# Optimization experiments

Measured on AMD Instinct MI355X. Metric: run time of the kernel, lower is better.

The kernel has to match this reference:

```python
import jax, jax.numpy as jnp
import numpy as np

D_MODEL = 2048
N_HEADS = 16
D_K = D_MODEL // N_HEADS
BATCH = 4
SEQ = 2048


def setup_inputs() -> dict:
    key = jax.random.key(0)
    ks = jax.random.split(key, 9)
    s = 1.0 / np.sqrt(D_MODEL)
    return {
        "x": jax.random.normal(ks[0], (BATCH, SEQ, D_MODEL), dtype=jnp.float32),
        "wq_w": jax.random.normal(ks[1], (D_MODEL, D_MODEL), dtype=jnp.float32) * s,
        "wq_b": jax.random.normal(ks[2], (D_MODEL,), dtype=jnp.float32) * 0.02,
        "wk_w": jax.random.normal(ks[3], (D_MODEL, D_MODEL), dtype=jnp.float32) * s,
        "wk_b": jax.random.normal(ks[4], (D_MODEL,), dtype=jnp.float32) * 0.02,
        "wv_w": jax.random.normal(ks[5], (D_MODEL, D_MODEL), dtype=jnp.float32) * s,
        "wv_b": jax.random.normal(ks[6], (D_MODEL,), dtype=jnp.float32) * 0.02,
        "wo_w": jax.random.normal(ks[7], (D_MODEL, D_MODEL), dtype=jnp.float32) * s,
        "wo_b": jax.random.normal(ks[8], (D_MODEL,), dtype=jnp.float32) * 0.02,
    }


def reference(x, wq_w, wq_b, wk_w, wk_b, wv_w, wv_b, wo_w, wo_b):
    b, s, _ = x.shape
    # Linear projections (torch Linear: x @ W^T + b)
    def split_heads(t):  # (b, s, d_model) -> (b, h, s, d_k)
        return t.reshape(b, s, N_HEADS, D_K).transpose(0, 2, 1, 3)
    q = split_heads(x @ wq_w.T + wq_b)
    k = split_heads(x @ wk_w.T + wk_b)
    v = split_heads(x @ wv_w.T + wv_b)
    scale = 1.0 / jnp.sqrt(jnp.asarray(D_K, dtype=x.dtype))
    scores = jnp.einsum("bhqd,bhkd->bhqk", q, k) * scale  # (b, h, s, s)
    attn = jax.nn.softmax(scores, axis=-1)
    ctx = jnp.einsum("bhqk,bhkd->bhqd", attn, v)
    ctx = ctx.transpose(0, 2, 1, 3).reshape(b, s, D_MODEL)
    out = ctx @ wo_w.T + wo_b
    return out
```

## Files before the change

kernel.cpp:

```cpp
#include <hip/hip_runtime.h>
#include <hip/hip_bf16.h>
#include <math.h>

typedef __attribute__((ext_vector_type(8))) short short8;
typedef __attribute__((ext_vector_type(4))) float f32x4;
typedef __attribute__((ext_vector_type(16))) float f32x16;
typedef __attribute__((ext_vector_type(4))) unsigned short u16x4;
typedef __attribute__((ext_vector_type(8))) unsigned short u16x8;
typedef __attribute__((ext_vector_type(4))) unsigned int u32x4;
typedef __attribute__((ext_vector_type(2))) int i32x2;
typedef unsigned short u16;
typedef unsigned int u32;

#define DM 2048
#define SQ 2048
#define NB 4
#define NH 16
#define DKH 128
#define KT 64
#define NT (SQ / KT)
#define LD3 (3 * DM)
#define QSCALE (0.08838834764831845f * 1.4426950408889634f)

__device__ __forceinline__ u16 f2bf(float f) {
  unsigned u = __float_as_uint(f);
  u += 0x7fffu + ((u >> 16) & 1u);
  return (u16)(u >> 16);
}

__device__ __forceinline__ u32 cvtpk(float lo, float hi) {
  u32 r;
  asm("v_cvt_pk_bf16_f32 %0, %1, %2" : "=v"(r) : "v"(lo), "v"(hi));
  return r;
}

__device__ __forceinline__ void gload16(const u16* g, u16* lds) {
  __builtin_amdgcn_global_load_lds(
      (const __attribute__((address_space(1))) unsigned int*)g,
      (__attribute__((address_space(3))) unsigned int*)lds, 16, 0, 0);
}

__global__ void cvt_bf16(const float* __restrict__ in, u16* __restrict__ out, int n) {
  int i = (blockIdx.x * blockDim.x + threadIdx.x) * 4;
  if (i >= n) return;
  float4 v = *(const float4*)(in + i);
  u16x4 o;
  o.x = f2bf(v.x); o.y = f2bf(v.y); o.z = f2bf(v.z); o.w = f2bf(v.w);
  *(u16x4*)(out + i) = o;
}

__global__ void cvt_w4(const float* __restrict__ w0, const float* __restrict__ w1,
                       const float* __restrict__ w2, const float* __restrict__ w3,
                       u16* __restrict__ dst) {
  const int sel = blockIdx.y;
  const float* src;
  switch (sel) {
    case 0: src = w0; break;
    case 1: src = w1; break;
    case 2: src = w2; break;
    default: src = w3; break;
  }
  const int i = (blockIdx.x * blockDim.x + threadIdx.x) * 4;
  float4 v = *(const float4*)(src + i);
  u16x4 o;
  o.x = f2bf(v.x); o.y = f2bf(v.y); o.z = f2bf(v.z); o.w = f2bf(v.w);
  *(u16x4*)(dst + (size_t)sel * DM * DM + i) = o;
}


#define STG_A(T, HALF)                                                     \
  do {                                                                     \
    _Pragma("unroll") for (int uu = 0; uu < 2; ++uu) {                     \
      const int j_ = w * 2 + uu;               \
      gload16(As + (size_t)((HALF) * 128 + (j_ >> 2) * 32) * K +           \
                  (size_t)(T) * 64 + (j_ & 3) * 16,                        \
              &smA[((T) & 1) * 16384 + ((HALF) * 16 + j_) * 512]);         \
    }                                                                      \
  } while (0)

#define STG_B(T, HALF)                                                     \
  do {                                                                     \
    _Pragma("unroll") for (int uu = 0; uu < 2; ++uu) {                     \
      const int j_ = w * 2 + uu;                                           \
      gload16(Bs + (size_t)((HALF) * 128 + (j_ >> 2) * 32) * K +           \
                  (size_t)(T) * 64 + (j_ & 3) * 16,                        \
              &smB[((T) & 1) * 16384 + ((HALF) * 16 + j_) * 512]);         \
    }                                                                      \
  } while (0)

#define LDA(QM)                                                            \
  do {                                                                     \
    const int rb_ = wr * 4 + (QM) * 2;                                     \
    const u16* p_ = &smA[bi * 16384 + rb_ * 2048 + l * 8];                 \
    _Pragma("unroll") for (int s = 0; s < 4; ++s) {                        \
      af[0][s] = *(const short8*)&p_[s * 512];                             \
      af[1][s] = *(const short8*)&p_[2048 + s * 512];                      \
    }                                                                      \
  } while (0)

#define LDB(QN)                                                            \
  do {                                                                     \
    const int rb_ = wc * 2 + (QN);                                         \
    const u16* p_ = &smB[bi * 16384 + rb_ * 2048 + l * 8];                 \
    _Pragma("unroll") for (int s = 0; s < 4; ++s)                          \
      bf[QN][s] = *(const short8*)&p_[s * 512];                            \
  } while (0)

#define MFMA_Q(QM, QN)                                                             \
  __builtin_amdgcn_s_setprio(1);                                                   \
  _Pragma("unroll") for (int s = 0; s < 4; ++s) {                                  \
    acc[(QM) * 2][(QN)] = __builtin_amdgcn_mfma_f32_32x32x16_bf16(                 \
        af[0][s], bf[QN][s], acc[(QM) * 2][(QN)], 0, 0, 0);                        \
    acc[(QM) * 2 + 1][(QN)] = __builtin_amdgcn_mfma_f32_32x32x16_bf16(             \
        af[1][s], bf[QN][s], acc[(QM) * 2 + 1][(QN)], 0, 0, 0);                    \
  }                                                                                \
  __builtin_amdgcn_s_setprio(0);

#define WAIT_LGKM                                         \
  asm volatile("s_waitcnt lgkmcnt(0)" ::: "memory");      \
  __builtin_amdgcn_sched_barrier(0);

template <int MODE>
__global__ __launch_bounds__(512, 2) void gemm8p(
    const u16* __restrict__ A, const u16* __restrict__ B,
    const float* __restrict__ bq, const float* __restrict__ bk,
    const float* __restrict__ bvp, void* __restrict__ Cout,
    int M, int N, int K) {
  __shared__ u16 smA[2 * 16384];
  __shared__ u16 smB[2 * 16384];
  const int tid = threadIdx.x;
  const int w = tid >> 6, l = tid & 63;
  const int c5 = l & 31, hi = l >> 5;
  const int wr = w >> 2, wc = w & 3;

  int flat = blockIdx.x + (int)gridDim.x * (int)blockIdx.y;
  const int nwg = (int)(gridDim.x * gridDim.y);
  flat = (flat & 7) * (nwg >> 3) + (flat >> 3);
  const int m0 = (flat / (int)gridDim.x) * 256, n0 = (flat % (int)gridDim.x) * 256;

  const int NSTEP = K / 64;
  f32x16 acc[4][2] = {};

  const u16* As = A + (size_t)(m0 + c5) * K + hi * 8;
  const u16* Bs = B + (size_t)(n0 + c5) * K + hi * 8;

  STG_A(0, 0); STG_A(0, 1); STG_B(0, 0); STG_B(0, 1);
  STG_B(1, 0); STG_A(1, 0);
  asm volatile("s_waitcnt vmcnt(4)" ::: "memory");
  __builtin_amdgcn_s_barrier();

  short8 af[2][4], bf[2][4];
  for (int t = 0; t < NSTEP; ++t) {
    const int bi = t & 1;
    LDA(0); LDB(0);
    if (t + 1 < NSTEP) STG_B(t + 1, 1);
    __builtin_amdgcn_s_barrier();
    WAIT_LGKM;
    MFMA_Q(0, 0);
    __builtin_amdgcn_s_barrier();
    LDB(1);
    if (t + 1 < NSTEP) STG_A(t + 1, 1);
    __builtin_amdgcn_s_barrier();
    WAIT_LGKM;
    MFMA_Q(0, 1);
    __builtin_amdgcn_s_barrier();
    LDA(1);
    if (t + 2 < NSTEP) STG_B(t + 2, 0);
    __builtin_amdgcn_s_barrier();
    WAIT_LGKM;
    MFMA_Q(1, 1);
    __builtin_amdgcn_s_barrier();
    if (t + 2 < NSTEP) STG_A(t + 2, 0);
    __builtin_amdgcn_s_barrier();
    MFMA_Q(1, 0);
    if (t + 2 < NSTEP)
      asm volatile("s_waitcnt vmcnt(4)" ::: "memory");
    else if (t + 1 < NSTEP)
      asm volatile("s_waitcnt vmcnt(0)" ::: "memory");
    __builtin_amdgcn_s_barrier();
  }

#pragma unroll
  for (int nf = 0; nf < 2; ++nf) {
    const int col = n0 + wc * 64 + nf * 32 + c5;
    float bval, os;
    if (MODE == 0) {
      const int seg = col >> 11;
      const float* bp = seg == 0 ? bq : (seg == 1 ? bk : bvp);
      bval = bp[col & (DM - 1)];
      os = (seg == 0) ? QSCALE : 1.0f;
    } else {
      bval = bq[col];
      os = 1.0f;
    }
#pragma unroll
    for (int mf = 0; mf < 4; ++mf) {
#pragma unroll
      for (int r = 0; r < 16; ++r) {
        const int row = m0 + wr * 128 + mf * 32 + (r & 3) + 8 * (r >> 2) + 4 * hi;
        const float v = (acc[mf][nf][r] + bval) * os;
        if (MODE == 1)
          ((float*)Cout)[(size_t)row * N + col] = v;
        else
          ((u16*)Cout)[(size_t)row * N + col] = f2bf(v);
      }
    }
  }
}

__global__ __launch_bounds__(512, 2) void attn(
    const u16* __restrict__ QKV, u16* __restrict__ O) {
  __shared__ u16 smK[2 * 8192];
  __shared__ u16 smV[9216];
  __shared__ float alScr[8 * 32];

  const u16* Qp = QKV;
  const u16* Kp = QKV + DM;
  const u16* Vp = QKV + 2 * DM;

  const int tid = threadIdx.x;
  const int w = tid >> 6, l = tid & 63;
  const int c5 = l & 31, hi = l >> 5;

  int flat = blockIdx.x + ((int)blockIdx.y << 3) + ((int)blockIdx.z << 7);
  flat = (flat & 7) * 64 + (flat >> 3);
  const int qt = flat & 7, h = (flat >> 3) & 15, b = flat >> 7;

  const int q0 = qt * 256 + w * 32;
  const size_t rowb = (size_t)b * SQ;
  const int hoff = h * DKH;

  short8 qf[8];
#pragma unroll
  for (int ds = 0; ds < 8; ++ds)
    qf[ds] = *(const short8*)&Qp[(rowb + q0 + c5) * LD3 + hoff + ds * 16 + hi * 8];

  f32x16 o[4] = {};
  float mrow = -1e30f, lsum = 0.f;

  const int vdg = tid >> 5;
  const int kvp = (tid & 31) * 2;
  u16x8 va, vb;

  {
#pragma unroll
    for (int uu = 0; uu < 2; ++uu) {
      const int u = w * 2 + uu;
      const int row = u * 4 + (l >> 4);
      const int col16 = (l & 15) ^ (row & 15);
      gload16(&Kp[(rowb + row) * LD3 + hoff + col16 * 8], &smK[u * 512]);
    }
    const u16* vp = &Vp[(rowb + kvp) * LD3 + hoff + vdg * 8];
    va = *(const u16x8*)vp;
    vb = *(const u16x8*)(vp + LD3);
#pragma unroll
    for (int i = 0; i < 8; ++i) {
      const int d = vdg * 8 + i;
      *(u32*)&smV[d * 72 + kvp] = (u32)va[i] | ((u32)vb[i] << 16);
    }
  }
  __syncthreads();

  int buf = 0;
  for (int t = 0; t < NT; ++t) {
    const int nb = buf ^ 1;
    if (t + 1 < NT) {
      const size_t kvr = rowb + (size_t)(t + 1) * KT;
#pragma unroll
      for (int uu = 0; uu < 2; ++uu) {
        const int u = w * 2 + uu;
        const int row = u * 4 + (l >> 4);
        const int col16 = (l & 15) ^ (row & 15);
        gload16(&Kp[(kvr + row) * LD3 + hoff + col16 * 8], &smK[nb * 8192 + u * 512]);
      }
      const u16* vp = &Vp[(kvr + kvp) * LD3 + hoff + vdg * 8];
      va = *(const u16x8*)vp;
      vb = *(const u16x8*)(vp + LD3);
    }

    f32x16 s[2] = {};
    __builtin_amdgcn_s_setprio(1);
#pragma unroll
    for (int ni = 0; ni < 2; ++ni) {
      const int row = ni * 32 + c5;
#pragma unroll
      for (int ds = 0; ds < 8; ++ds) {
        const short8 kf = *(const short8*)&smK[buf * 8192 + row * 128 + (((ds << 1) | hi) ^ (row & 15)) * 8];
        s[ni] = __builtin_amdgcn_mfma_f32_32x32x16_bf16(kf, qf[ds], s[ni], 0, 0, 0);
      }
    }
    __builtin_amdgcn_s_setprio(0);

    float mx = s[0][0];
#pragma unroll
    for (int ni = 0; ni < 2; ++ni)
#pragma unroll
      for (int i = 0; i < 16; ++i)
        mx = fmaxf(mx, s[ni][i]);
    i32x2 sw = __builtin_amdgcn_permlane32_swap(__float_as_int(mx), __float_as_int(mx), false, false);
    const float gmax = fmaxf(__int_as_float(sw.x), __int_as_float(sw.y));

    if (__any(gmax > mrow + 10.0f)) {
      const float mn = fmaxf(mrow, gmax);
      const float al = exp2f(mrow - mn);
      mrow = mn;
      lsum *= al;
      alScr[w * 32 + c5] = al;
#pragma unroll
      for (int r = 0; r < 16; ++r) {
        const float av = alScr[w * 32 + (r & 3) + 8 * (r >> 2) + 4 * hi];
#pragma unroll
        for (int dg = 0; dg < 4; ++dg) o[dg][r] *= av;
      }
    }

    float ps0 = 0.f, ps1 = 0.f;
#pragma unroll
    for (int i = 0; i < 16; ++i) {
      const float p0 = exp2f(s[0][i] - mrow);
      const float p1 = exp2f(s[1][i] - mrow);
      s[0][i] = p0; s[1][i] = p1;
      ps0 += p0; ps1 += p1;
    }
    lsum += ps0 + ps1;

    __builtin_amdgcn_s_setprio(1);
#pragma unroll
    for (int ks = 0; ks < 4; ++ks) {
      const int b0 = (ks & 1) * 8;
      const int ni = ks >> 1;
      const u32 A0 = cvtpk(s[ni][b0 + 0], s[ni][b0 + 1]);
      const u32 A1 = cvtpk(s[ni][b0 + 4], s[ni][b0 + 5]);
      const u32 B0 = cvtpk(s[ni][b0 + 2], s[ni][b0 + 3]);
      const u32 B1 = cvtpk(s[ni][b0 + 6], s[ni][b0 + 7]);
      const i32x2 r0 = __builtin_amdgcn_permlane32_swap((int)A0, (int)A1, false, false);
      const i32x2 r1 = __builtin_amdgcn_permlane32_swap((int)B0, (int)B1, false, false);
      u32x4 paw;
      paw.x = (u32)r0.x; paw.y = (u32)r1.x; paw.z = (u32)r0.y; paw.w = (u32)r1.y;
      const short8 pa = *(const short8*)&paw;
#pragma unroll
      for (int dg = 0; dg < 4; ++dg) {
        const int rowd = dg * 32 + c5;
        const short8 vf = *(const short8*)&smV[rowd * 72 + ks * 16 + hi * 8];
        o[dg] = __builtin_amdgcn_mfma_f32_32x32x16_bf16(pa, vf, o[dg], 0, 0, 0);
      }
    }
    __builtin_amdgcn_s_setprio(0);

    __syncthreads();
    if (t + 1 < NT) {
#pragma unroll
      for (int i = 0; i < 8; ++i) {
        const int d = vdg * 8 + i;
        *(u32*)&smV[d * 72 + kvp] = (u32)va[i] | ((u32)vb[i] << 16);
      }
      __syncthreads();
    }
    buf = nb;
  }

  {
    const i32x2 sl = __builtin_amdgcn_permlane32_swap(__float_as_int(lsum), __float_as_int(lsum), false, false);
    const float tot = __int_as_float(sl.x) + __int_as_float(sl.y);
    alScr[w * 32 + c5] = 1.0f / tot;
  }
#pragma unroll
  for (int r = 0; r < 16; ++r) {
    const int qloc = (r & 3) + 8 * (r >> 2) + 4 * hi;
    const float inv = alScr[w * 32 + qloc];
    const size_t orow = (rowb + q0 + qloc) * DM + hoff;
#pragma unroll
    for (int dg = 0; dg < 4; ++dg)
      O[orow + dg * 32 + c5] = f2bf(o[dg][r] * inv);
  }
}

extern "C" void kernel_launch(void* const* d_in, const int* in_sizes, int n_in,
                              void* d_out, int out_size, void* d_ws, size_t ws_size,
                              hipStream_t stream) {
  const float* x    = (const float*)d_in[0];
  const float* wq_w = (const float*)d_in[1];
  const float* wq_b = (const float*)d_in[2];
  const float* wk_w = (const float*)d_in[3];
  const float* wk_b = (const float*)d_in[4];
  const float* wv_w = (const float*)d_in[5];
  const float* wv_b = (const float*)d_in[6];
  const float* wo_w = (const float*)d_in[7];
  const float* wo_b = (const float*)d_in[8];
  float* out = (float*)d_out;

  u16* p = (u16*)d_ws;
  u16* xb  = p; p += (size_t)NB * SQ * DM;
  u16* wqb = p; p += (size_t)3 * DM * DM;
  u16* wob = p; p += (size_t)DM * DM;
  u16* QKV = p; p += (size_t)NB * SQ * 3 * DM;
  u16* ctx = xb;

  const int nx = NB * SQ * DM;
  cvt_bf16<<<dim3(nx / 1024), dim3(256), 0, stream>>>(x, xb, nx);
  cvt_w4<<<dim3(DM * DM / 1024, 4), dim3(256), 0, stream>>>(wq_w, wk_w, wv_w, wo_w, wqb);

  dim3 gg3(3 * DM / 256, (NB * SQ) / 256);
  gemm8p<0><<<gg3, dim3(512), 0, stream>>>(xb, wqb, wq_b, wk_b, wv_b, QKV,
                                           NB * SQ, 3 * DM, DM);

  attn<<<dim3(SQ / 256, NH, NB), dim3(512), 0, stream>>>(QKV, ctx);

  dim3 ggo(DM / 256, (NB * SQ) / 256);
  gemm8p<1><<<ggo, dim3(512), 0, stream>>>(ctx, wob, wo_b, nullptr, nullptr, out,
                                           NB * SQ, DM, DM);
}
```

Baseline: 573.2 us.

## Pre-tile GEMM operands into LDS-chunk order during bf16 conversion

The fp32-to-bf16 conversion kernels, and the attention output store, now write operands in a blocked layout that matches the GEMM's LDS staging chunks, so each global_load_lds reads one contiguous 1KB chunk instead of strided rows. This is meant to improve global-load coalescing and cut address arithmetic in the GEMM main loops. In exchange, the attention context stores become scattered 2-byte writes through a computed address. The conversion kernels also move to 8-element stores.

```diff
diff --git a/kernel.cpp b/kernel.cpp
--- a/kernel.cpp
+++ b/kernel.cpp
@@ -40,18 +40,27 @@
       (__attribute__((address_space(3))) unsigned int*)lds, 16, 0, 0);
 }
 
-__global__ void cvt_bf16(const float* __restrict__ in, u16* __restrict__ out, int n) {
-  int i = (blockIdx.x * blockDim.x + threadIdx.x) * 4;
-  if (i >= n) return;
-  float4 v = *(const float4*)(in + i);
-  u16x4 o;
-  o.x = f2bf(v.x); o.y = f2bf(v.y); o.z = f2bf(v.z); o.w = f2bf(v.w);
-  *(u16x4*)(out + i) = o;
-}
-
-__global__ void cvt_w4(const float* __restrict__ w0, const float* __restrict__ w1,
-                       const float* __restrict__ w2, const float* __restrict__ w3,
-                       u16* __restrict__ dst) {
+__device__ __forceinline__ int paddr16(int r, int k, int nkt) {
+  const int cid = (((r >> 8) * nkt + (k >> 6)) << 5) | (((r >> 7) & 1) << 4) |
+                  (((r >> 5) & 3) << 2) | ((k >> 4) & 3);
+  return (cid << 9) + (((r & 31) | (((k >> 3) & 1) << 5)) << 3) + (k & 7);
+}
+
+__global__ void cvt_x_p(const float* __restrict__ in, u16* __restrict__ out) {
+  const int idx = blockIdx.x * 256 + threadIdx.x;
+  const int r = idx >> 8;
+  const int k = (idx & 255) << 3;
+  const float4 v0 = *(const float4*)(in + (size_t)r * DM + k);
+  const float4 v1 = *(const float4*)(in + (size_t)r * DM + k + 4);
+  u16x8 o;
+  o[0] = f2bf(v0.x); o[1] = f2bf(v0.y); o[2] = f2bf(v0.z); o[3] = f2bf(v0.w);
+  o[4] = f2bf(v1.x); o[5] = f2bf(v1.y); o[6] = f2bf(v1.z); o[7] = f2bf(v1.w);
+  *(u16x8*)(out + paddr16(r, k, 32)) = o;
+}
+
+__global__ void cvt_w_p(const float* __restrict__ w0, const float* __restrict__ w1,
+                        const float* __restrict__ w2, const float* __restrict__ w3,
+                        u16* __restrict__ dq, u16* __restrict__ dw) {
   const int sel = blockIdx.y;
   const float* src;
   switch (sel) {
@@ -60,32 +69,37 @@
     case 2: src = w2; break;
     default: src = w3; break;
   }
-  const int i = (blockIdx.x * blockDim.x + threadIdx.x) * 4;
-  float4 v = *(const float4*)(src + i);
-  u16x4 o;
-  o.x = f2bf(v.x); o.y = f2bf(v.y); o.z = f2bf(v.z); o.w = f2bf(v.w);
-  *(u16x4*)(dst + (size_t)sel * DM * DM + i) = o;
-}
-
-
-#define STG_A(T, HALF)                                                     \
-  do {                                                                     \
-    _Pragma("unroll") for (int uu = 0; uu < 2; ++uu) {                     \
-      const int j_ = w * 2 + uu;               \
-      gload16(As + (size_t)((HALF) * 128 + (j_ >> 2) * 32) * K +           \
-                  (size_t)(T) * 64 + (j_ & 3) * 16,                        \
-              &smA[((T) & 1) * 16384 + ((HALF) * 16 + j_) * 512]);         \
-    }                                                                      \
+  const int idx = blockIdx.x * 256 + threadIdx.x;
+  const int r = idx >> 8;
+  const int k = (idx & 255) << 3;
+  const float4 v0 = *(const float4*)(src + (size_t)r * DM + k);
+  const float4 v1 = *(const float4*)(src + (size_t)r * DM + k + 4);
+  u16x8 o;
+  o[0] = f2bf(v0.x); o[1] = f2bf(v0.y); o[2] = f2bf(v0.z); o[3] = f2bf(v0.w);
+  o[4] = f2bf(v1.x); o[5] = f2bf(v1.y); o[6] = f2bf(v1.z); o[7] = f2bf(v1.w);
+  if (sel < 3)
+    *(u16x8*)(dq + paddr16(sel * DM + r, k, 32)) = o;
+  else
+    *(u16x8*)(dw + paddr16(r, k, 32)) = o;
+}
+
+
+#define STG_A(T, HALF)                                                       \
+  do {                                                                       \
+    _Pragma("unroll") for (int uu = 0; uu < 2; ++uu) {                       \
+      const int j_ = w * 2 + uu;                                             \
+      gload16(As + ((((T) * 32 + (HALF) * 16 + j_) << 9) + l * 8),           \
+              &smA[((T) & 1) * 16384 + ((HALF) * 16 + j_) * 512]);           \
+    }                                                                        \
   } while (0)
 
-#define STG_B(T, HALF)                                                     \
-  do {                                                                     \
-    _Pragma("unroll") for (int uu = 0; uu < 2; ++uu) {                     \
-      const int j_ = w * 2 + uu;                                           \
-      gload16(Bs + (size_t)((HALF) * 128 + (j_ >> 2) * 32) * K +           \
-                  (size_t)(T) * 64 + (j_ & 3) * 16,                        \
-              &smB[((T) & 1) * 16384 + ((HALF) * 16 + j_) * 512]);         \
-    }                                                                      \
+#define STG_B(T, HALF)                                                       \
+  do {                                                                       \
+    _Pragma("unroll") for (int uu = 0; uu < 2; ++uu) {                       \
+      const int j_ = w * 2 + uu;                                             \
+      gload16(Bs + ((((T) * 32 + (HALF) * 16 + j_) << 9) + l * 8),           \
+              &smB[((T) & 1) * 16384 + ((HALF) * 16 + j_) * 512]);           \
+    }                                                                        \
   } while (0)
 
 #define LDA(QM)                                                            \
@@ -141,8 +155,8 @@
   const int NSTEP = K / 64;
   f32x16 acc[4][2] = {};
 
-  const u16* As = A + (size_t)(m0 + c5) * K + hi * 8;
-  const u16* Bs = B + (size_t)(n0 + c5) * K + hi * 8;
+  const u16* As = A + (size_t)(m0 >> 8) * NSTEP * 16384;
+  const u16* Bs = B + (size_t)(n0 >> 8) * NSTEP * 16384;
 
   STG_A(0, 0); STG_A(0, 1); STG_B(0, 0); STG_B(0, 1);
   STG_B(1, 0); STG_A(1, 0);
@@ -368,10 +382,10 @@
   for (int r = 0; r < 16; ++r) {
     const int qloc = (r & 3) + 8 * (r >> 2) + 4 * hi;
     const float inv = alScr[w * 32 + qloc];
-    const size_t orow = (rowb + q0 + qloc) * DM + hoff;
+    const int rowg = (int)rowb + q0 + qloc;
 #pragma unroll
     for (int dg = 0; dg < 4; ++dg)
-      O[orow + dg * 32 + c5] = f2bf(o[dg][r] * inv);
+      O[paddr16(rowg, hoff + dg * 32 + c5, 32)] = f2bf(o[dg][r] * inv);
   }
 }
 
@@ -396,9 +410,8 @@
   u16* QKV = p; p += (size_t)NB * SQ * 3 * DM;
   u16* ctx = xb;
 
-  const int nx = NB * SQ * DM;
-  cvt_bf16<<<dim3(nx / 1024), dim3(256), 0, stream>>>(x, xb, nx);
-  cvt_w4<<<dim3(DM * DM / 1024, 4), dim3(256), 0, stream>>>(wq_w, wk_w, wv_w, wo_w, wqb);
+  cvt_x_p<<<dim3(NB * SQ * DM / 2048), dim3(256), 0, stream>>>(x, xb);
+  cvt_w_p<<<dim3(DM * DM / 2048, 4), dim3(256), 0, stream>>>(wq_w, wk_w, wv_w, wo_w, wqb, wob);
 
   dim3 gg3(3 * DM / 256, (NB * SQ) / 256);
   gemm8p<0><<<gg3, dim3(512), 0, stream>>>(xb, wqb, wq_b, wk_b, wv_b, QKV,
```

Result: slower. 587.7 us (+2.5%).
